# Performance work log

Hardware: AMD Instinct MI355X
Metric: run time of the kernel (lower is better)

Reference implementation:

```python
import jax, jax.numpy as jnp
import numpy as np
import math

B, S, D = 16, 1024, 2048  # batch, seq_len, feats_size; LSTM hidden H = D
H = D

def setup_inputs() -> dict:
    key = jax.random.key(0)
    ks = jax.random.split(key, 12)
    s = 1.0 / math.sqrt(D)
    return {
        "feats": jax.random.normal(ks[0], (B, S, D), jnp.float32),
        "Wq": jax.random.normal(ks[1], (D, D), jnp.float32) * s,
        "bq": jnp.zeros((D,), jnp.float32),
        "Wk": jax.random.normal(ks[2], (D, D), jnp.float32) * s,
        "bk": jnp.zeros((D,), jnp.float32),
        "Wv": jax.random.normal(ks[3], (D, D), jnp.float32) * s,
        "bv": jnp.zeros((D,), jnp.float32),
        "W_ih": jax.random.normal(ks[4], (4 * H, D), jnp.float32) * s,
        "W_hh": jax.random.normal(ks[5], (4 * H, H), jnp.float32) * s,
        "b_ih": jnp.zeros((4 * H,), jnp.float32),
        "b_hh": jnp.zeros((4 * H,), jnp.float32),
    }

def _lstm(x, W_ih, W_hh, b_ih, b_hh):
    # x: [B, S, D] -> hidden sequence [B, S, H]. torch nn.LSTM gate order i,f,g,o.
    xg = jnp.einsum('bsd,gd->bsg', x, W_ih) + b_ih + b_hh  # [B,S,4H], input part precomputed
    xg = jnp.swapaxes(xg, 0, 1)  # [S,B,4H] for scan over time
    h0 = jnp.zeros((x.shape[0], H), x.dtype)
    c0 = jnp.zeros((x.shape[0], H), x.dtype)
    def step(carry, xt):
        h, c = carry
        gates = xt + h @ W_hh.T  # [B,4H]
        i, f, g, o = jnp.split(gates, 4, axis=-1)
        c = jax.nn.sigmoid(f) * c + jax.nn.sigmoid(i) * jnp.tanh(g)
        h = jax.nn.sigmoid(o) * jnp.tanh(c)
        return (h, c), h
    _, hs = jax.lax.scan(step, (h0, c0), xg)
    return jnp.swapaxes(hs, 0, 1)  # [B,S,H]

def reference(feats, Wq, bq, Wk, bk, Wv, bv, W_ih, W_hh, b_ih, b_hh):
    q = feats @ Wq.T + bq
    k = feats @ Wk.T + bk
    v = feats @ Wv.T + bv
    dot = jnp.einsum('bsd,btd->bst', q, k) / math.sqrt(2048.0)
    w = jax.nn.softmax(dot, axis=-1)
    new_feats = jnp.einsum('bst,btd->bsd', w, v)
    return _lstm(new_feats, W_ih, W_hh, b_ih, b_hh)
```

## Files before the change

### kernel.cpp

```cpp
#include <hip/hip_runtime.h>


typedef unsigned short u16;
typedef unsigned int u32;
typedef unsigned long long u64;
typedef __attribute__((ext_vector_type(8))) __bf16 bf16x8;
typedef __attribute__((ext_vector_type(8))) unsigned short u16x8;
typedef __attribute__((ext_vector_type(4))) float f32x4;
typedef __attribute__((ext_vector_type(4))) unsigned int u32x4;

#define DEV static __device__ __forceinline__

DEV u16 f2bf(float f) {
  union { float f; unsigned u; } x; x.f = f;
  return (u16)((x.u + 0x7FFFu + ((x.u >> 16) & 1u)) >> 16);
}
DEV float bf2f(u16 h) {
  union { unsigned u; float f; } x; x.u = (unsigned)h << 16;
  return x.f;
}
DEV void gload_lds16(const void* g, void* l) {
  __builtin_amdgcn_global_load_lds(
      (const __attribute__((address_space(1))) unsigned int*)g,
      (__attribute__((address_space(3))) unsigned int*)l, 16, 0, 0);
}

__global__ __launch_bounds__(256) void k_cvt(const float* __restrict__ in,
                                             u16* __restrict__ out, long n) {
  long i = (((long)blockIdx.x << 8) | threadIdx.x) << 3;
  if (i >= n) return;
  float4 f0 = *(const float4*)(in + i);
  float4 f1 = *(const float4*)(in + i + 4);
  u16x8 p;
  p[0] = f2bf(f0.x); p[1] = f2bf(f0.y); p[2] = f2bf(f0.z); p[3] = f2bf(f0.w);
  p[4] = f2bf(f1.x); p[5] = f2bf(f1.y); p[6] = f2bf(f1.z); p[7] = f2bf(f1.w);
  *(u16x8*)(out + i) = p;
}

__global__ __launch_bounds__(256) void k_addb(const float* __restrict__ a,
                                              const float* __restrict__ b,
                                              float* __restrict__ o, int n) {
  int i = blockIdx.x * 256 + threadIdx.x;
  if (i < n) o[i] = a[i] + b[i];
}

template<int OBF>
__global__ __launch_bounds__(512, 2) void k_gemm256(
    const u16* __restrict__ A, const u16* __restrict__ B, void* __restrict__ Cv,
    const float* __restrict__ bias, float scale, int N, int K,
    long sA, long sB, long sC) {
  extern __shared__ u16 lds[];
  u16* As = lds;
  u16* Bs = lds + 32768;
  const int tid = threadIdx.x;
  const int lane = tid & 63, wid = tid >> 6;
  const int wm = (wid >> 2) & 1, wn = wid & 3;
  const int gx = gridDim.x;
  int lin = blockIdx.y * gx + blockIdx.x;
  const int nwg = gx * gridDim.y;
  if ((nwg & 7) == 0) lin = (lin & 7) * (nwg >> 3) + (lin >> 3);
  const long bm = (long)(lin / gx) << 8;
  const long bn = (long)(lin % gx) << 8;
  A += (long)blockIdx.z * sA;
  B += (long)blockIdx.z * sB;
  const int NK = K >> 5;

  u32 srow[2], scolb[2];
#pragma unroll
  for (int p = 0; p < 2; ++p) {
    const u32 q = (u32)(p * 8192 + tid * 16);
    const u32 qp = q ^ (((q >> 9) & 1u) << 5);
    srow[p] = qp >> 6; scolb[p] = qp & 63u;
  }
#define STAGE256(S, KT)                                                      \
  {                                                                          \
    _Pragma("unroll")                                                        \
    for (int p = 0; p < 2; ++p) {                                            \
      const u32 q = (u32)(p * 8192 + tid * 16);                              \
      gload_lds16(A + (bm + srow[p]) * (long)K + (KT) * 32 + (scolb[p] >> 1),\
                  (char*)As + (S) * 16384 + q);                              \
      gload_lds16(B + (bn + srow[p]) * (long)K + (KT) * 32 + (scolb[p] >> 1),\
                  (char*)Bs + (S) * 16384 + q);                              \
    }                                                                        \
  }

  const int fr = lane & 15, fkb = ((lane >> 4) << 3) << 1;
  u32 abyte[8], bbyte[4];
#pragma unroll
  for (int mi = 0; mi < 8; ++mi) {
    const u32 row = (u32)(wm * 128 + mi * 16 + fr);
    abyte[mi] = (row * 64 + (u32)fkb) ^ ((row & 8u) ? 32u : 0u);
  }
#pragma unroll
  for (int ni = 0; ni < 4; ++ni) {
    const u32 row = (u32)(wn * 64 + ni * 16 + fr);
    bbyte[ni] = (row * 64 + (u32)fkb) ^ ((row & 8u) ? 32u : 0u);
  }

  f32x4 acc[8][4] = {};
#define COMPUTE256(SLOT)                                                     \
  {                                                                          \
    const char* sa = (const char*)As + (SLOT) * 16384;                       \
    const char* sb = (const char*)Bs + (SLOT) * 16384;                       \
    bf16x8 av[8], bv[4];                                                     \
    _Pragma("unroll")                                                        \
    for (int mi = 0; mi < 8; ++mi) av[mi] = *(const bf16x8*)(sa + abyte[mi]);\
    _Pragma("unroll")                                                        \
    for (int ni = 0; ni < 4; ++ni) bv[ni] = *(const bf16x8*)(sb + bbyte[ni]);\
    asm volatile("s_waitcnt lgkmcnt(0)" ::: "memory");                       \
    __builtin_amdgcn_s_barrier();                                            \
    __builtin_amdgcn_s_setprio(1);                                           \
    _Pragma("unroll")                                                        \
    for (int mi = 0; mi < 8; ++mi)                                           \
      _Pragma("unroll")                                                      \
      for (int ni = 0; ni < 4; ++ni)                                         \
        acc[mi][ni] = __builtin_amdgcn_mfma_f32_16x16x32_bf16(               \
            av[mi], bv[ni], acc[mi][ni], 0, 0, 0);                           \
    __builtin_amdgcn_s_setprio(0);                                           \
  }

  STAGE256(0, 0)
  STAGE256(1, 1)
  STAGE256(2, 2)
  int kt = 0;
  for (; kt < NK - 3; ++kt) {
    STAGE256((kt + 3) & 3, kt + 3)
    asm volatile("s_waitcnt vmcnt(12)" ::: "memory");
    __builtin_amdgcn_s_barrier();
    COMPUTE256(kt & 3)
  }
  asm volatile("s_waitcnt vmcnt(8)" ::: "memory");
  __builtin_amdgcn_s_barrier();
  COMPUTE256(kt & 3) ++kt;
  asm volatile("s_waitcnt vmcnt(4)" ::: "memory");
  __builtin_amdgcn_s_barrier();
  COMPUTE256(kt & 3) ++kt;
  asm volatile("s_waitcnt vmcnt(0)" ::: "memory");
  __builtin_amdgcn_s_barrier();
  COMPUTE256(kt & 3)
#undef STAGE256
#undef COMPUTE256

  const long cb = (long)blockIdx.z * sC;
#pragma unroll
  for (int ni = 0; ni < 4; ++ni) {
    const long col = bn + wn * 64 + ni * 16 + fr;
    const float bb = bias ? bias[col] : 0.f;
#pragma unroll
    for (int mi = 0; mi < 8; ++mi) {
      const long r0 = bm + wm * 128 + mi * 16 + ((lane >> 4) << 2);
#pragma unroll
      for (int r = 0; r < 4; ++r) {
        const float v = acc[mi][ni][r] * scale + bb;
        const long off = cb + (r0 + r) * (long)N + col;
        if (OBF) ((u16*)Cv)[off] = f2bf(v);
        else     ((float*)Cv)[off] = v;
      }
    }
  }
}

__global__ __launch_bounds__(256) void k_softmax(const float* __restrict__ S,
                                                 u16* __restrict__ P) {
  __shared__ float red[8];
  const long row = blockIdx.x;
  const float* sr = S + (row << 10);
  const int t = threadIdx.x, lane = t & 63, w = t >> 6;
  float v0 = sr[t], v1 = sr[t + 256], v2 = sr[t + 512], v3 = sr[t + 768];
  float m = fmaxf(fmaxf(v0, v1), fmaxf(v2, v3));
#pragma unroll
  for (int o = 32; o; o >>= 1) m = fmaxf(m, __shfl_xor(m, o));
  if (lane == 0) red[w] = m;
  __syncthreads();
  m = fmaxf(fmaxf(red[0], red[1]), fmaxf(red[2], red[3]));
  v0 = __expf(v0 - m); v1 = __expf(v1 - m); v2 = __expf(v2 - m); v3 = __expf(v3 - m);
  float s = v0 + v1 + v2 + v3;
#pragma unroll
  for (int o = 32; o; o >>= 1) s += __shfl_xor(s, o);
  if (lane == 0) red[4 + w] = s;
  __syncthreads();
  s = red[4] + red[5] + red[6] + red[7];
  const float rs = 1.f / s;
  u16* pr = P + (row << 10);
  pr[t] = f2bf(v0 * rs); pr[t + 256] = f2bf(v1 * rs);
  pr[t + 512] = f2bf(v2 * rs); pr[t + 768] = f2bf(v3 * rs);
}

__global__ __launch_bounds__(256) void k_transpose(const u16* __restrict__ V,
                                                   u16* __restrict__ VT) {
  __shared__ __attribute__((aligned(16))) u16 tile[64][80];
  const long b = blockIdx.z;
  const long t0 = (long)blockIdx.y << 6, d0 = (long)blockIdx.x << 6;
  const int r = threadIdx.x >> 3, c8 = (threadIdx.x & 7) << 3;
  const u16* src = V + ((b << 10) + t0) * 2048 + d0;
#pragma unroll
  for (int p = 0; p < 2; ++p) {
    const int rr = r + p * 32;
    *(u16x8*)&tile[rr][c8] = *(const u16x8*)(src + (long)rr * 2048 + c8);
  }
  __syncthreads();
  u16* dst = VT + ((b << 11) + d0) * 1024 + t0;
#pragma unroll
  for (int p = 0; p < 2; ++p) {
    const int dr = r + p * 32;
    u16x8 pk;
#pragma unroll
    for (int q = 0; q < 8; ++q) pk[q] = tile[c8 + q][dr];
    *(u16x8*)(dst + (long)dr * 1024 + c8) = pk;
  }
}

DEV bf16x8 wread(const char* wlds, int nrow, int k) {
  int byte = (nrow << 12) + (k << 1);
  byte ^= (nrow & 7) << 4;
  return *(const bf16x8*)(wlds + byte);
}
DEV float sigm(float x) { return 1.f / (1.f + __expf(-x)); }
DEV float tanh_fast(float x) { return 1.f - 2.f / (1.f + __expf(2.f * x)); }

__global__ __launch_bounds__(256, 1) void k_lstm(
    const u16* __restrict__ xg, const u16* __restrict__ whh,
    u16* __restrict__ hbuf, float* __restrict__ out,
    unsigned* __restrict__ flg) {
  extern __shared__ char smem[];
  char* wlds = smem;
  float* red = (float*)(smem + 131072);
  const int tid = threadIdx.x, lane = tid & 63, wave = tid >> 6;
  const int j0 = blockIdx.x << 4;
  const int am = lane & 15, ak = (lane >> 4) << 3;
  const int bb = tid >> 4, jj = tid & 15;

  for (int it = 0; it < 32; ++it) {
    const long grow = ((long)(it >> 4) << 11) + j0 + (it & 15);
    const u16* src = whh + grow * 2048 + (tid << 3);
    int byte = (it << 12) + (tid << 4);
    byte ^= (it & 7) << 4;
    *(bf16x8*)(wlds + byte) = *(const bf16x8*)src;
  }
  bf16x8 wf[2][16];
#pragma unroll
  for (int g2 = 0; g2 < 2; ++g2)
#pragma unroll
    for (int ks = 0; ks < 16; ++ks)
      wf[g2][ks] = *(const bf16x8*)(whh + ((long)((2 + g2) << 11) + j0 + am) * 2048 +
                                    (wave << 9) + (ks << 5) + ak);
  __syncthreads();

  float c = 0.f;
  unsigned* const myflag = flg + (((wave << 5) + (lane & 31)) << 2);
  u16 xv[4];
#pragma unroll
  for (int g = 0; g < 4; ++g)
    xv[g] = xg[((long)bb << 10) * 8192 + (g << 11) + j0 + jj];

  for (int t = 0; t < 1024; ++t) {
    const int par = t & 1;
    unsigned dep = 0;
    if (t) {
      const unsigned tgt = (unsigned)t;
      unsigned v = tgt;
      for (;;) {
        if (lane < 32)
          v = __hip_atomic_load(myflag, __ATOMIC_RELAXED, __HIP_MEMORY_SCOPE_AGENT);
        if (__all(v >= tgt)) break;
        __builtin_amdgcn_s_sleep(1);
      }
      dep = v >> 20;
    }
    asm volatile("" : "+v"(dep)::);

    const u16* hbase = hbuf + ((par ^ 1) << 15);
    const u32 voff = ((am << 11) + (wave << 9) + ak + dep) << 1;
    u32x4 hd[16];
#define HLD(I, OFF)                                                          \
    asm volatile("global_load_dwordx4 %0, %1, %2 offset:" #OFF " sc0 sc1"    \
                 : "=v"(hd[I]) : "v"(voff), "s"(hbase));
    HLD(0, 0)    HLD(1, 64)   HLD(2, 128)  HLD(3, 192)
    HLD(4, 256)  HLD(5, 320)  HLD(6, 384)  HLD(7, 448)
    HLD(8, 512)  HLD(9, 576)  HLD(10, 640) HLD(11, 704)
    HLD(12, 768) HLD(13, 832) HLD(14, 896) HLD(15, 960)
#undef HLD
    asm volatile("s_waitcnt vmcnt(0)" ::: "memory");
    __builtin_amdgcn_sched_barrier(0);

    f32x4 a0 = {0.f, 0.f, 0.f, 0.f}, a1 = a0, a2 = a0, a3 = a0;
#pragma unroll
    for (int ks = 0; ks < 16; ++ks) {
      union { u32x4 d; bf16x8 v; } u;
      u.d = hd[ks];
      const int k = (wave << 9) + (ks << 5) + ak;
      a0 = __builtin_amdgcn_mfma_f32_16x16x32_bf16(u.v, wread(wlds, am, k),      a0, 0, 0, 0);
      a1 = __builtin_amdgcn_mfma_f32_16x16x32_bf16(u.v, wread(wlds, am + 16, k), a1, 0, 0, 0);
      a2 = __builtin_amdgcn_mfma_f32_16x16x32_bf16(u.v, wf[0][ks], a2, 0, 0, 0);
      a3 = __builtin_amdgcn_mfma_f32_16x16x32_bf16(u.v, wf[1][ks], a3, 0, 0, 0);
    }
    {
      float* rw = red + (wave << 10);
      const int mrow = (lane >> 4) << 2;
#pragma unroll
      for (int r = 0; r < 4; ++r) {
        rw[(mrow + r) * 64 + am]      = a0[r];
        rw[(mrow + r) * 64 + 16 + am] = a1[r];
        rw[(mrow + r) * 64 + 32 + am] = a2[r];
        rw[(mrow + r) * 64 + 48 + am] = a3[r];
      }
    }
    __syncthreads();
    float g4[4];
#pragma unroll
    for (int g = 0; g < 4; ++g) {
      const int n = (bb << 6) + (g << 4) + jj;
      g4[g] = red[n] + red[1024 + n] + red[2048 + n] + red[3072 + n] + bf2f(xv[g]);
    }
    const float gi = sigm(g4[0]);
    const float gf = sigm(g4[1]);
    const float gg = tanh_fast(g4[2]);
    const float go = sigm(g4[3]);
    c = gf * c + gi * gg;
    const float h = go * tanh_fast(c);
    {
      const unsigned hb = (unsigned)f2bf(h);
      const unsigned p1 = (unsigned)__shfl_xor((int)hb, 1);
      const unsigned w2 = (hb & 0xFFFFu) | (p1 << 16);
      const unsigned p2 = (unsigned)__shfl_xor((int)w2, 2);
      if ((jj & 3) == 0) {
        const u64 hw = (u64)w2 | ((u64)p2 << 32);
        u16* dst = hbuf + (par << 15) + (bb << 11) + j0 + jj;
        __hip_atomic_store((u64*)dst, hw, __ATOMIC_RELAXED, __HIP_MEMORY_SCOPE_AGENT);
      }
    }
    asm volatile("s_waitcnt vmcnt(0)" ::: "memory");
    __syncthreads();
    if (tid == 0)
      __hip_atomic_store(flg + (blockIdx.x << 2), (unsigned)(t + 1),
                         __ATOMIC_RELAXED, __HIP_MEMORY_SCOPE_AGENT);
    out[(((long)(bb << 10) + t) << 11) + j0 + jj] = h;
    {
      const int tn = (t + 1 < 1024) ? t + 1 : 0;
#pragma unroll
      for (int g = 0; g < 4; ++g)
        xv[g] = xg[((long)((bb << 10) + tn)) * 8192 + (g << 11) + j0 + jj];
    }
    asm volatile("" ::: "memory");
  }
}

extern "C" void kernel_launch(void* const* d_in, const int* in_sizes, int n_in,
                              void* d_out, int out_size, void* d_ws, size_t ws_size,
                              hipStream_t stream) {
  const float* feats = (const float*)d_in[0];
  const float* Wq = (const float*)d_in[1];
  const float* bq = (const float*)d_in[2];
  const float* Wk = (const float*)d_in[3];
  const float* bk = (const float*)d_in[4];
  const float* Wv = (const float*)d_in[5];
  const float* bv = (const float*)d_in[6];
  const float* Wih = (const float*)d_in[7];
  const float* Whh = (const float*)d_in[8];
  const float* bih = (const float*)d_in[9];
  const float* bhh = (const float*)d_in[10];
  float* out = (float*)d_out;
  char* ws = (char*)d_ws;

  u16* feats16 = (u16*)(ws + 0L);
  u16* q16     = (u16*)(ws + 67108864L);
  u16* k16     = (u16*)(ws + 134217728L);
  u16* v16     = (u16*)(ws + 201326592L);
  u16* vT16    = feats16;
  u16* P16     = q16;
  u16* xg16    = (u16*)(ws + 0L);
  u16* nf16    = (u16*)(ws + 268435456L);
  u16* wq16    = (u16*)(ws + 335544320L);
  u16* wk16    = (u16*)(ws + 343932928L);
  u16* wv16    = (u16*)(ws + 352321536L);
  u16* wih16   = (u16*)(ws + 360710144L);
  u16* whh16   = (u16*)(ws + 394264576L);
  float* biassum = (float*)(ws + 427819008L);
  u16* hbuf    = (u16*)(ws + 427851776L);
  unsigned* flg = (unsigned*)(ws + 427982848L);
  float* scoresf = (float*)d_out;

  k_cvt<<<16384, 256, 0, stream>>>(feats, feats16, 33554432L);
  k_cvt<<<2048, 256, 0, stream>>>(Wq, wq16, 4194304L);
  k_cvt<<<2048, 256, 0, stream>>>(Wk, wk16, 4194304L);
  k_cvt<<<2048, 256, 0, stream>>>(Wv, wv16, 4194304L);
  k_cvt<<<8192, 256, 0, stream>>>(Wih, wih16, 16777216L);
  k_cvt<<<8192, 256, 0, stream>>>(Whh, whh16, 16777216L);
  k_addb<<<32, 256, 0, stream>>>(bih, bhh, biassum, 8192);

  (void)hipFuncSetAttribute((const void*)k_gemm256<1>, hipFuncAttributeMaxDynamicSharedMemorySize, 131072);
  (void)hipFuncSetAttribute((const void*)k_gemm256<0>, hipFuncAttributeMaxDynamicSharedMemorySize, 131072);
  k_gemm256<1><<<dim3(8, 64, 1), 512, 131072, stream>>>(feats16, wq16, q16, bq, 1.f, 2048, 2048, 0, 0, 0);
  k_gemm256<1><<<dim3(8, 64, 1), 512, 131072, stream>>>(feats16, wk16, k16, bk, 1.f, 2048, 2048, 0, 0, 0);
  k_gemm256<1><<<dim3(8, 64, 1), 512, 131072, stream>>>(feats16, wv16, v16, bv, 1.f, 2048, 2048, 0, 0, 0);
  k_gemm256<0><<<dim3(4, 4, 16), 512, 131072, stream>>>(q16, k16, scoresf, nullptr,
                                                        0.022097086912079608f, 1024, 2048,
                                                        2097152, 2097152, 1048576);
  k_softmax<<<16384, 256, 0, stream>>>(scoresf, P16);
  k_transpose<<<dim3(32, 16, 16), 256, 0, stream>>>(v16, vT16);
  k_gemm256<1><<<dim3(8, 4, 16), 512, 131072, stream>>>(P16, vT16, nf16, nullptr, 1.f,
                                                        2048, 1024,
                                                        1048576, 2097152, 2097152);
  k_gemm256<1><<<dim3(32, 64, 1), 512, 131072, stream>>>(nf16, wih16, xg16, biassum, 1.f, 8192, 2048, 0, 0, 0);

  hipMemsetAsync(ws + 427851776L, 0, 131072 + 4096, stream);
  const int dynlds = 131072 + 16384;
  (void)hipFuncSetAttribute((const void*)k_lstm, hipFuncAttributeMaxDynamicSharedMemorySize, dynlds);
  void* kargs[] = {(void*)&xg16, (void*)&whh16, (void*)&hbuf, (void*)&out, (void*)&flg};
  hipError_t ce = hipLaunchCooperativeKernel((const void*)k_lstm, dim3(128), dim3(256),
                                             kargs, dynlds, stream);
  if (ce != hipSuccess) {
    k_lstm<<<dim3(128), dim3(256), dynlds, stream>>>(xg16, whh16, hbuf, out, flg);
  }
}
```

Measured before the change: 6.681 ms.

## Double-buffer LDS fragment reads across k-tiles to overlap with MFMAs

Restructures the GEMM main loop so fragments for the next k-tile are read from LDS into a second register set while the MFMAs for the current tile run, with the loop unrolled by two to alternate buffers. The goal is to hide LDS read latency behind matrix-core work instead of waiting on lgkmcnt before each MFMA block. In exchange it doubles fragment register usage, which can lower occupancy or cause spills, and the loop now steps by two, so the trip count is only correct for certain NK values.

```diff
diff --git a/kernel.cpp b/kernel.cpp
--- a/kernel.cpp
+++ b/kernel.cpp
@@ -98,48 +98,75 @@
   }
 
   f32x4 acc[8][4] = {};
-#define COMPUTE256(SLOT)                                                     \
+  bf16x8 avA[8], bvA[4], avB[8], bvB[4];
+#define READF(AV, BV, SLOT)                                                  \
   {                                                                          \
     const char* sa = (const char*)As + (SLOT) * 16384;                       \
     const char* sb = (const char*)Bs + (SLOT) * 16384;                       \
-    bf16x8 av[8], bv[4];                                                     \
     _Pragma("unroll")                                                        \
-    for (int mi = 0; mi < 8; ++mi) av[mi] = *(const bf16x8*)(sa + abyte[mi]);\
+    for (int mi = 0; mi < 8; ++mi) AV[mi] = *(const bf16x8*)(sa + abyte[mi]);\
     _Pragma("unroll")                                                        \
-    for (int ni = 0; ni < 4; ++ni) bv[ni] = *(const bf16x8*)(sb + bbyte[ni]);\
-    asm volatile("s_waitcnt lgkmcnt(0)" ::: "memory");                       \
-    __builtin_amdgcn_s_barrier();                                            \
+    for (int ni = 0; ni < 4; ++ni) BV[ni] = *(const bf16x8*)(sb + bbyte[ni]);\
+  }
+#define MFMAS(AV, BV)                                                        \
+  {                                                                          \
     __builtin_amdgcn_s_setprio(1);                                           \
     _Pragma("unroll")                                                        \
     for (int mi = 0; mi < 8; ++mi)                                           \
       _Pragma("unroll")                                                      \
       for (int ni = 0; ni < 4; ++ni)                                         \
         acc[mi][ni] = __builtin_amdgcn_mfma_f32_16x16x32_bf16(               \
-            av[mi], bv[ni], acc[mi][ni], 0, 0, 0);                           \
+            AV[mi], BV[ni], acc[mi][ni], 0, 0, 0);                           \
     __builtin_amdgcn_s_setprio(0);                                           \
   }
+#define VMC(N) asm volatile("s_waitcnt vmcnt(" #N ")" ::: "memory");
+#define LGK0   asm volatile("s_waitcnt lgkmcnt(0)" ::: "memory");
 
   STAGE256(0, 0)
   STAGE256(1, 1)
   STAGE256(2, 2)
+  VMC(8)
+  __builtin_amdgcn_s_barrier();
+  READF(avA, bvA, 0)
+  LGK0
+
   int kt = 0;
-  for (; kt < NK - 3; ++kt) {
+  for (; kt < NK - 4; kt += 2) {
     STAGE256((kt + 3) & 3, kt + 3)
-    asm volatile("s_waitcnt vmcnt(12)" ::: "memory");
+    VMC(8)
     __builtin_amdgcn_s_barrier();
-    COMPUTE256(kt & 3)
-  }
-  asm volatile("s_waitcnt vmcnt(8)" ::: "memory");
+    READF(avB, bvB, (kt + 1) & 3)
+    MFMAS(avA, bvA)
+    LGK0
+    STAGE256((kt + 4) & 3, kt + 4)
+    VMC(8)
+    __builtin_amdgcn_s_barrier();
+    READF(avA, bvA, (kt + 2) & 3)
+    MFMAS(avB, bvB)
+    LGK0
+  }
+  STAGE256((NK - 1) & 3, NK - 1)
+  VMC(8)
   __builtin_amdgcn_s_barrier();
-  COMPUTE256(kt & 3) ++kt;
-  asm volatile("s_waitcnt vmcnt(4)" ::: "memory");
+  READF(avB, bvB, (NK - 3) & 3)
+  MFMAS(avA, bvA)
+  LGK0
+  VMC(4)
   __builtin_amdgcn_s_barrier();
-  COMPUTE256(kt & 3) ++kt;
-  asm volatile("s_waitcnt vmcnt(0)" ::: "memory");
+  READF(avA, bvA, (NK - 2) & 3)
+  MFMAS(avB, bvB)
+  LGK0
+  VMC(0)
   __builtin_amdgcn_s_barrier();
-  COMPUTE256(kt & 3)
+  READF(avB, bvB, (NK - 1) & 3)
+  MFMAS(avA, bvA)
+  LGK0
+  MFMAS(avB, bvB)
 #undef STAGE256
-#undef COMPUTE256
+#undef READF
+#undef MFMAS
+#undef VMC
+#undef LGK0
 
   const long cb = (long)blockIdx.z * sC;
 #pragma unroll
```

Result: slower. 7.274 ms (+8.9%).
